# Performance work log

Hardware: AMD Instinct MI355X
Metric: run time of the kernel (lower is better)

## Reference

```python
import jax, jax.numpy as jnp
import numpy as np

B, T, QD, KD, E, H, L = 4, 512, 256, 256, 256, 8, 4
DH = E // H
SHAPES = np.array([[64, 64], [32, 32], [16, 16], [8, 8]], dtype=np.int64)
S = int(np.sum(SHAPES[:, 0] * SHAPES[:, 1]))  # 5440


def setup_inputs() -> dict:
    key = jax.random.key(0)
    ks = jax.random.split(key, 16)
    std = 0.02
    return {
        "q": jax.random.normal(ks[0], (B, T, QD), jnp.float32),
        "k": jax.random.normal(ks[1], (B, S, KD), jnp.float32),
        "v": jax.random.normal(ks[2], (B, S, KD), jnp.float32),
        "Wq": jax.random.normal(ks[3], (E, QD), jnp.float32) * std,
        "bq": jnp.zeros((E,), jnp.float32),
        "Wk": jax.random.normal(ks[4], (E, KD), jnp.float32) * std,
        "bk": jnp.zeros((E,), jnp.float32),
        "Wv": jax.random.normal(ks[5], (E, KD), jnp.float32) * std,
        "bv": jnp.zeros((E,), jnp.float32),
        "Wo": jax.random.normal(ks[6], (QD, E), jnp.float32) * std,
        "bo": jnp.zeros((QD,), jnp.float32),
        "Wl": jax.random.normal(ks[7], (H * L, QD), jnp.float32) * std,
        "bl": jnp.zeros((H * L,), jnp.float32),
        "k_spatial_shapes": SHAPES,  # static int metadata (split sizes)
    }


def _heads(x, b):
    # [b, s, E] -> [b, H, s, DH]
    return x.reshape(b, -1, H, DH).transpose(0, 2, 1, 3)


def reference(q, k, v, Wq, bq, Wk, bk, Wv, bv, Wo, bo, Wl, bl, k_spatial_shapes):
    scale = DH ** -0.5
    bsz = q.shape[0]
    # per-head, per-level gate: [B, H, T, L], softmax over levels
    gates = jax.nn.softmax(
        (q @ Wl.T + bl).reshape(bsz, -1, H, L).transpose(0, 2, 1, 3), axis=-1
    )
    qs = _heads((q @ Wq.T + bq) * scale, bsz)   # [B,H,T,DH]
    ks_ = _heads(k @ Wk.T + bk, bsz)            # [B,H,S,DH]
    vs = _heads(v @ Wv.T + bv, bsz)             # [B,H,S,DH]
    scores = jnp.einsum("bhtd,bhsd->bhts", qs, ks_)  # [B,H,T,S]
    sizes = [int(h_ * w_) for h_, w_ in np.asarray(k_spatial_shapes)]
    offs = np.concatenate([[0], np.cumsum(sizes)])
    # segmented softmax per level, weighted by the learned level gate
    pieces = [
        jax.nn.softmax(scores[..., offs[i]:offs[i + 1]], axis=-1) * gates[..., i:i + 1]
        for i in range(len(sizes))
    ]
    attn = jnp.concatenate(pieces, axis=-1)  # [B,H,T,S]
    out = jnp.einsum("bhts,bhsd->bhtd", attn, vs)
    out = out.transpose(0, 2, 1, 3).reshape(bsz, -1, E)
    out = out @ Wo.T + bo
    return out, attn
```

## Files before the change

kernel.cpp:

```cpp
#include <hip/hip_runtime.h>
#include <hip/hip_bf16.h>

#define Bn 4
#define Hn 8
#define Tn 512
#define Sn 5440
#define DHn 32
#define En 256

typedef short bf16x8 __attribute__((ext_vector_type(8)));
typedef float f32x4 __attribute__((ext_vector_type(4)));

static __device__ __forceinline__ unsigned short f2bf(float f) {
    union { float f; unsigned u; } c; c.f = f;
    unsigned r = c.u + 0x7fffu + ((c.u >> 16) & 1u);
    return (unsigned short)(r >> 16);
}

static __device__ __forceinline__ unsigned int cvtpk(float a, float b) {
    __hip_bfloat162 h = __float22bfloat162_rn(make_float2(a, b));
    unsigned int u; __builtin_memcpy(&u, &h, 4); return u;
}

__global__ __launch_bounds__(256) void gates_kernel(
    const float* __restrict__ q, const float* __restrict__ Wl,
    const float* __restrict__ bl, float* __restrict__ gates)
{
    __shared__ float qr[8][256];
    __shared__ float lgs[8][32];
    int tid = threadIdx.x;
    int bt0 = blockIdx.x * 8;

    {
        const float4* src = (const float4*)(q + (size_t)bt0 * 256);
        float4* dst = (float4*)&qr[0][0];
        dst[tid] = src[tid];
        dst[tid + 256] = src[tid + 256];
    }
    __syncthreads();

    int r = tid >> 5, o = tid & 31;
    float acc = 0.f;
    const float4* w4 = (const float4*)(Wl + (size_t)o * 256);
    const float4* q4 = (const float4*)&qr[r][0];
    #pragma unroll 8
    for (int i = 0; i < 64; i++) {
        float4 w = w4[i]; float4 qq = q4[i];
        acc += qq.x*w.x + qq.y*w.y + qq.z*w.z + qq.w*w.w;
    }
    lgs[r][o] = acc + bl[o];
    __syncthreads();

    if (tid < 64) {
        int rr = tid >> 3, h = tid & 7;
        float x0 = lgs[rr][h*4+0], x1 = lgs[rr][h*4+1], x2 = lgs[rr][h*4+2], x3 = lgs[rr][h*4+3];
        float mx = fmaxf(fmaxf(x0,x1), fmaxf(x2,x3));
        float e0 = __expf(x0-mx), e1 = __expf(x1-mx), e2 = __expf(x2-mx), e3 = __expf(x3-mx);
        float inv = 1.f / (e0+e1+e2+e3);
        int bt = bt0 + rr; int b = bt >> 9, t = bt & 511;
        float* g = gates + (((size_t)b*Hn + h)*Tn + t)*4;
        g[0] = e0*inv; g[1] = e1*inv; g[2] = e2*inv; g[3] = e3*inv;
    }
}

static __device__ __forceinline__ void gemm_core(
    const float* __restrict__ A, const float* __restrict__ W,
    int row0, int col0, int tid, int wr, int wc, int lr, int lg,
    unsigned short (*As)[40], unsigned short (*Ws)[40], f32x4 acc[4][4])
{
    for (int k0 = 0; k0 < 256; k0 += 32) {
        __syncthreads();
        #pragma unroll
        for (int i = 0; i < 4; i++) {
            int f4 = tid + i*256;
            int r = f4 >> 3, kc = (f4 & 7) * 4;
            float4 v = *(const float4*)(A + (size_t)(row0 + r)*256 + k0 + kc);
            uint2 pk; pk.x = cvtpk(v.x, v.y); pk.y = cvtpk(v.z, v.w);
            *(uint2*)&As[r][kc] = pk;
        }
        #pragma unroll
        for (int i = 0; i < 4; i++) {
            int f4 = tid + i*256;
            int r = f4 >> 3, kc = (f4 & 7) * 4;
            float4 v = *(const float4*)(W + (size_t)(col0 + r)*256 + k0 + kc);
            uint2 pk; pk.x = cvtpk(v.x, v.y); pk.y = cvtpk(v.z, v.w);
            *(uint2*)&Ws[r][kc] = pk;
        }
        __syncthreads();

        bf16x8 af[4], wf[4];
        #pragma unroll
        for (int i = 0; i < 4; i++) {
            af[i] = *(const bf16x8*)&As[wr*64 + i*16 + lr][lg*8];
            wf[i] = *(const bf16x8*)&Ws[wc*64 + i*16 + lr][lg*8];
        }
        #pragma unroll
        for (int i = 0; i < 4; i++)
            #pragma unroll
            for (int j = 0; j < 4; j++)
                acc[i][j] = __builtin_amdgcn_mfma_f32_16x16x32_bf16(af[i], wf[j], acc[i][j], 0, 0, 0);
    }
}

__global__ __launch_bounds__(256) void proj_kvq(
    const float* __restrict__ kin, const float* __restrict__ Wk, const float* __restrict__ bk,
    const float* __restrict__ vin, const float* __restrict__ Wv, const float* __restrict__ bv,
    const float* __restrict__ qin, const float* __restrict__ Wq, const float* __restrict__ bq,
    unsigned short* __restrict__ ks_out, unsigned short* __restrict__ vt_out,
    unsigned short* __restrict__ qs_out)
{
    int mode = blockIdx.z;
    if (mode == 2 && blockIdx.x >= 16) return;

    __shared__ unsigned short As[128][40];
    __shared__ unsigned short Ws[128][40];

    const float* A    = (mode == 0) ? kin : (mode == 1) ? vin : qin;
    const float* W    = (mode == 0) ? Wk  : (mode == 1) ? Wv  : Wq;
    const float* bias = (mode == 0) ? bk  : (mode == 1) ? bv  : bq;

    int tid = threadIdx.x;
    int l = tid & 63, wid = tid >> 6;
    int wr = wid >> 1, wc = wid & 1;
    int lr = l & 15, lg = l >> 4;
    int row0 = blockIdx.x * 128, col0 = blockIdx.y * 128;

    f32x4 acc[4][4] = {};
    gemm_core(A, W, row0, col0, tid, wr, wc, lr, lg, As, Ws, acc);

    const float qscale = 0.17677669529663687f * 1.4426950408889634f;

    #pragma unroll
    for (int i = 0; i < 4; i++) {
        int m0 = row0 + wr*64 + i*16 + lg*4;
        #pragma unroll
        for (int j = 0; j < 4; j++) {
            int col = col0 + wc*64 + j*16 + lr;
            float bvv = bias[col];
            if (mode == 0) {
                #pragma unroll
                for (int r = 0; r < 4; r++) {
                    int m = m0 + r;
                    int b = m / Sn, s = m - b*Sn;
                    ks_out[(((size_t)b*Hn + (col >> 5))*Sn + s)*DHn + (col & 31)] = f2bf(acc[i][j][r] + bvv);
                }
            } else if (mode == 1) {
                int b = m0 / Sn, s0 = m0 - b*Sn;
                uint2 pk;
                pk.x = cvtpk(acc[i][j][0] + bvv, acc[i][j][1] + bvv);
                pk.y = cvtpk(acc[i][j][2] + bvv, acc[i][j][3] + bvv);
                *(uint2*)&vt_out[(((size_t)b*Hn + (col >> 5))*DHn + (col & 31))*Sn + s0] = pk;
            } else {
                #pragma unroll
                for (int r = 0; r < 4; r++) {
                    int m = m0 + r;
                    int b = m >> 9, t = m & 511;
                    qs_out[(((size_t)b*Hn + (col >> 5))*Tn + t)*DHn + (col & 31)] = f2bf((acc[i][j][r] + bvv) * qscale);
                }
            }
        }
    }
}

__global__ __launch_bounds__(256) void proj_out(
    const float* __restrict__ A, const float* __restrict__ W,
    const float* __restrict__ bias, float* __restrict__ out)
{
    __shared__ unsigned short As[128][40];
    __shared__ unsigned short Ws[128][40];

    int tid = threadIdx.x;
    int l = tid & 63, wid = tid >> 6;
    int wr = wid >> 1, wc = wid & 1;
    int lr = l & 15, lg = l >> 4;
    int row0 = blockIdx.x * 128, col0 = blockIdx.y * 128;

    f32x4 acc[4][4] = {};
    gemm_core(A, W, row0, col0, tid, wr, wc, lr, lg, As, Ws, acc);

    #pragma unroll
    for (int i = 0; i < 4; i++) {
        int m0 = row0 + wr*64 + i*16 + lg*4;
        #pragma unroll
        for (int j = 0; j < 4; j++) {
            int col = col0 + wc*64 + j*16 + lr;
            float bvv = bias[col];
            #pragma unroll
            for (int r = 0; r < 4; r++)
                __builtin_nontemporal_store(acc[i][j][r] + bvv, &out[(size_t)(m0 + r)*256 + col]);
        }
    }
}

__global__ __launch_bounds__(256, 5) void attn_fused(
    const unsigned short* __restrict__ qs, const unsigned short* __restrict__ ks,
    const unsigned short* __restrict__ vt, const float* __restrict__ gates,
    float* __restrict__ attn_out, float* __restrict__ o_tmp)
{
    __shared__ char plds[4][2048];
    __shared__ char estw[4][4096];
    __shared__ float lsum[4][4][16];
    __shared__ float denom[4][16];

    int n = blockIdx.x;
    int bh = ((n >> 8) << 3) | (n & 7);
    int tt = (n >> 3) & 31;
    int t0 = tt << 4;
    int b = bh >> 3, h = bh & 7;
    int tid = threadIdx.x;
    int l = tid & 63, w = tid >> 6;
    int lr = l & 15, lg = l >> 4;

    bf16x8 aq = *(const bf16x8*)(qs + ((size_t)bh*Tn + t0 + lr)*DHn + lg*8);
    const unsigned short* kb = ks + (size_t)bh * Sn * DHn;
    const unsigned short* vb = vt + (size_t)bh * DHn * Sn;
    const f32x4 fzero = {0.f, 0.f, 0.f, 0.f};

    float lp0 = 0.f, lp1 = 0.f, lp2 = 0.f, lp3 = 0.f;
    for (int c = w; c < 85; c += 4) {
        const unsigned short* kc_ = kb + (size_t)c * 64 * DHn;
        bf16x8 kf0 = *(const bf16x8*)(kc_ + (size_t)(lr     )*DHn + lg*8);
        bf16x8 kf1 = *(const bf16x8*)(kc_ + (size_t)(16 + lr)*DHn + lg*8);
        bf16x8 kf2 = *(const bf16x8*)(kc_ + (size_t)(32 + lr)*DHn + lg*8);
        bf16x8 kf3 = *(const bf16x8*)(kc_ + (size_t)(48 + lr)*DHn + lg*8);
        f32x4 s0 = __builtin_amdgcn_mfma_f32_16x16x32_bf16(kf0, aq, fzero, 0, 0, 0);
        f32x4 s1 = __builtin_amdgcn_mfma_f32_16x16x32_bf16(kf1, aq, fzero, 0, 0, 0);
        f32x4 s2 = __builtin_amdgcn_mfma_f32_16x16x32_bf16(kf2, aq, fzero, 0, 0, 0);
        f32x4 s3 = __builtin_amdgcn_mfma_f32_16x16x32_bf16(kf3, aq, fzero, 0, 0, 0);
        float es = exp2f(s0[0]) + exp2f(s0[1]) + exp2f(s0[2]) + exp2f(s0[3])
                 + exp2f(s1[0]) + exp2f(s1[1]) + exp2f(s1[2]) + exp2f(s1[3])
                 + exp2f(s2[0]) + exp2f(s2[1]) + exp2f(s2[2]) + exp2f(s2[3])
                 + exp2f(s3[0]) + exp2f(s3[1]) + exp2f(s3[2]) + exp2f(s3[3]);
        if      (c < 64) lp0 += es;
        else if (c < 80) lp1 += es;
        else if (c < 84) lp2 += es;
        else             lp3 += es;
    }
    {
        float v;
        v = lp0; v += __shfl_xor(v, 16); v += __shfl_xor(v, 32); lp0 = v;
        v = lp1; v += __shfl_xor(v, 16); v += __shfl_xor(v, 32); lp1 = v;
        v = lp2; v += __shfl_xor(v, 16); v += __shfl_xor(v, 32); lp2 = v;
        v = lp3; v += __shfl_xor(v, 16); v += __shfl_xor(v, 32); lp3 = v;
    }
    if (l < 16) {
        lsum[w][0][lr] = lp0; lsum[w][1][lr] = lp1;
        lsum[w][2][lr] = lp2; lsum[w][3][lr] = lp3;
    }
    __syncthreads();
    if (tid < 64) {
        int seg = tid >> 4, row = tid & 15;
        denom[seg][row] = lsum[0][seg][row] + lsum[1][seg][row] + lsum[2][seg][row] + lsum[3][seg][row];
    }
    __syncthreads();

    float lcf0, lcf1, lcf2, lcf3;
    {
        const float* g = gates + ((size_t)bh*Tn + t0 + lr)*4;
        lcf0 = __log2f(g[0] / denom[0][lr]);
        lcf1 = __log2f(g[1] / denom[1][lr]);
        lcf2 = __log2f(g[2] / denom[2][lr]);
        lcf3 = __log2f(g[3] / denom[3][lr]);
    }

    f32x4 acc0 = fzero, acc1 = fzero;
    char* pbase = plds[w];
    char* ebase = estw[w];
    int swz = (lr & 7) << 4;
    float* abase = attn_out + ((size_t)bh*Tn + t0)*Sn;

    for (int c = w; c < 85; c += 4) {
        float lcf = (c < 64) ? lcf0 : (c < 80) ? lcf1 : (c < 84) ? lcf2 : lcf3;

        const unsigned short* kc_ = kb + (size_t)c * 64 * DHn;
        bf16x8 kf0 = *(const bf16x8*)(kc_ + (size_t)(lr     )*DHn + lg*8);
        bf16x8 kf1 = *(const bf16x8*)(kc_ + (size_t)(16 + lr)*DHn + lg*8);
        bf16x8 kf2 = *(const bf16x8*)(kc_ + (size_t)(32 + lr)*DHn + lg*8);
        bf16x8 kf3 = *(const bf16x8*)(kc_ + (size_t)(48 + lr)*DHn + lg*8);
        bf16x8 vf0 = *(const bf16x8*)(vb + (size_t)(lr     )*Sn + c*64      + lg*8);
        bf16x8 vf1 = *(const bf16x8*)(vb + (size_t)(16 + lr)*Sn + c*64      + lg*8);
        bf16x8 vf2 = *(const bf16x8*)(vb + (size_t)(lr     )*Sn + c*64 + 32 + lg*8);
        bf16x8 vf3 = *(const bf16x8*)(vb + (size_t)(16 + lr)*Sn + c*64 + 32 + lg*8);

        f32x4 s0 = __builtin_amdgcn_mfma_f32_16x16x32_bf16(kf0, aq, fzero, 0, 0, 0);
        f32x4 s1 = __builtin_amdgcn_mfma_f32_16x16x32_bf16(kf1, aq, fzero, 0, 0, 0);
        f32x4 s2 = __builtin_amdgcn_mfma_f32_16x16x32_bf16(kf2, aq, fzero, 0, 0, 0);
        f32x4 s3 = __builtin_amdgcn_mfma_f32_16x16x32_bf16(kf3, aq, fzero, 0, 0, 0);

        {
            f32x4 av;
            av[0] = exp2f(s0[0]+lcf); av[1] = exp2f(s0[1]+lcf); av[2] = exp2f(s0[2]+lcf); av[3] = exp2f(s0[3]+lcf);
            *(f32x4*)(ebase + ((lr*256 +   0 + lg*16) ^ swz)) = av;
            uint2 pk; pk.x = cvtpk(av[0], av[1]); pk.y = cvtpk(av[2], av[3]);
            *(uint2*)(pbase + ((lr*128 +   0 + lg*8) ^ swz)) = pk;
            av[0] = exp2f(s1[0]+lcf); av[1] = exp2f(s1[1]+lcf); av[2] = exp2f(s1[2]+lcf); av[3] = exp2f(s1[3]+lcf);
            *(f32x4*)(ebase + ((lr*256 +  64 + lg*16) ^ swz)) = av;
            pk.x = cvtpk(av[0], av[1]); pk.y = cvtpk(av[2], av[3]);
            *(uint2*)(pbase + ((lr*128 +  32 + lg*8) ^ swz)) = pk;
            av[0] = exp2f(s2[0]+lcf); av[1] = exp2f(s2[1]+lcf); av[2] = exp2f(s2[2]+lcf); av[3] = exp2f(s2[3]+lcf);
            *(f32x4*)(ebase + ((lr*256 + 128 + lg*16) ^ swz)) = av;
            pk.x = cvtpk(av[0], av[1]); pk.y = cvtpk(av[2], av[3]);
            *(uint2*)(pbase + ((lr*128 +  64 + lg*8) ^ swz)) = pk;
            av[0] = exp2f(s3[0]+lcf); av[1] = exp2f(s3[1]+lcf); av[2] = exp2f(s3[2]+lcf); av[3] = exp2f(s3[3]+lcf);
            *(f32x4*)(ebase + ((lr*256 + 192 + lg*16) ^ swz)) = av;
            pk.x = cvtpk(av[0], av[1]); pk.y = cvtpk(av[2], av[3]);
            *(uint2*)(pbase + ((lr*128 +  96 + lg*8) ^ swz)) = pk;
        }

        __builtin_amdgcn_s_setprio(1);
        {
            bf16x8 pa0 = *(const bf16x8*)(pbase + ((lr*128 +      lg*16) ^ swz));
            acc0 = __builtin_amdgcn_mfma_f32_16x16x32_bf16(pa0, vf0, acc0, 0, 0, 0);
            acc1 = __builtin_amdgcn_mfma_f32_16x16x32_bf16(pa0, vf1, acc1, 0, 0, 0);
            bf16x8 pa1 = *(const bf16x8*)(pbase + ((lr*128 + 64 + lg*16) ^ swz));
            acc0 = __builtin_amdgcn_mfma_f32_16x16x32_bf16(pa1, vf2, acc0, 0, 0, 0);
            acc1 = __builtin_amdgcn_mfma_f32_16x16x32_bf16(pa1, vf3, acc1, 0, 0, 0);
        }
        __builtin_amdgcn_s_setprio(0);

        #pragma unroll
        for (int i = 0; i < 4; i++) {
            int row = i*4 + lg;
            f32x4 vv = *(const f32x4*)(ebase + ((row*256 + lr*16) ^ ((row & 7) << 4)));
            __builtin_nontemporal_store(vv, (f32x4*)(abase + (size_t)row*Sn + c*64 + lr*4));
        }
    }

    float* ored = (float*)estw[w];
    #pragma unroll
    for (int r = 0; r < 4; r++) {
        ored[(4*lg + r)*32 + lr]      = acc0[r];
        ored[(4*lg + r)*32 + 16 + lr] = acc1[r];
    }
    __syncthreads();
    #pragma unroll
    for (int i = 0; i < 2; i++) {
        int idx = tid + i*256;
        int row = idx >> 5, d = idx & 31;
        float sum = ((float*)estw[0])[row*32 + d] + ((float*)estw[1])[row*32 + d]
                  + ((float*)estw[2])[row*32 + d] + ((float*)estw[3])[row*32 + d];
        __builtin_nontemporal_store(sum, &o_tmp[((size_t)(b*Tn + t0 + row))*En + h*DHn + d]);
    }
}

extern "C" void kernel_launch(void* const* d_in, const int* in_sizes, int n_in,
                              void* d_out, int out_size, void* d_ws, size_t ws_size,
                              hipStream_t stream)
{
    const float* q  = (const float*)d_in[0];
    const float* k  = (const float*)d_in[1];
    const float* v  = (const float*)d_in[2];
    const float* Wq = (const float*)d_in[3];
    const float* bq = (const float*)d_in[4];
    const float* Wk = (const float*)d_in[5];
    const float* bk = (const float*)d_in[6];
    const float* Wv = (const float*)d_in[7];
    const float* bv = (const float*)d_in[8];
    const float* Wo = (const float*)d_in[9];
    const float* bo = (const float*)d_in[10];
    const float* Wl = (const float*)d_in[11];
    const float* bl = (const float*)d_in[12];

    float* out  = (float*)d_out;
    float* attn = out + (size_t)Bn*Tn*256;

    char* ws = (char*)d_ws;
    unsigned short* qs    = (unsigned short*)ws;
    unsigned short* ksb   = (unsigned short*)(ws + (1u<<20));
    unsigned short* vtb   = (unsigned short*)(ws + (1u<<20) + 11141120u);
    float*          gates = (float*)(ws + (1u<<20) + 2u*11141120u);
    float*          o_tmp = (float*)(ws + (1u<<20) + 2u*11141120u + 262144u);

    gates_kernel<<<Bn*Tn/8, 256, 0, stream>>>(q, Wl, bl, gates);
    proj_kvq<<<dim3((Bn*Sn)/128, 2, 3), 256, 0, stream>>>(
        k, Wk, bk, v, Wv, bv, q, Wq, bq, ksb, vtb, qs);
    attn_fused<<<Bn*Hn*(Tn/16), 256, 0, stream>>>(qs, ksb, vtb, gates, attn, o_tmp);
    proj_out<<<dim3((Bn*Tn)/128, 2), 256, 0, stream>>>(o_tmp, Wo, bo, out);
}
```

Measured before the change: 160.8 us.

## Process two 16-row query tiles per block to reuse K/V loads

Each attention block now handles 32 query rows instead of 16, sharing each loaded K and V fragment across two MFMA query tiles. This halves global K/V fragment traffic and halves the grid size. In exchange it doubles LDS staging and register use, drops the occupancy hint from launch bounds, and leaves fewer blocks to spread across CUs.

```diff
diff --git a/kernel.cpp b/kernel.cpp
--- a/kernel.cpp
+++ b/kernel.cpp
@@ -192,85 +192,110 @@
     }
 }
 
-__global__ __launch_bounds__(256, 5) void attn_fused(
+__global__ __launch_bounds__(256) void attn_fused(
     const unsigned short* __restrict__ qs, const unsigned short* __restrict__ ks,
     const unsigned short* __restrict__ vt, const float* __restrict__ gates,
     float* __restrict__ attn_out, float* __restrict__ o_tmp)
 {
-    __shared__ char plds[4][2048];
-    __shared__ char estw[4][4096];
-    __shared__ float lsum[4][4][16];
-    __shared__ float denom[4][16];
+    __shared__ char plds[4][2][2048];
+    __shared__ char estw[4][2][4096];
+    __shared__ float lsum[4][2][4][16];
+    __shared__ float denom[2][4][16];
 
     int n = blockIdx.x;
-    int bh = ((n >> 8) << 3) | (n & 7);
-    int tt = (n >> 3) & 31;
-    int t0 = tt << 4;
+    int xcd = n & 7, j = n >> 3;
+    int bh = ((j >> 4) << 3) | xcd;
+    int t0 = (j & 15) << 5;
     int b = bh >> 3, h = bh & 7;
     int tid = threadIdx.x;
     int l = tid & 63, w = tid >> 6;
     int lr = l & 15, lg = l >> 4;
 
-    bf16x8 aq = *(const bf16x8*)(qs + ((size_t)bh*Tn + t0 + lr)*DHn + lg*8);
+    bf16x8 aqA = *(const bf16x8*)(qs + ((size_t)bh*Tn + t0 + lr)*DHn + lg*8);
+    bf16x8 aqB = *(const bf16x8*)(qs + ((size_t)bh*Tn + t0 + 16 + lr)*DHn + lg*8);
     const unsigned short* kb = ks + (size_t)bh * Sn * DHn;
     const unsigned short* vb = vt + (size_t)bh * DHn * Sn;
     const f32x4 fzero = {0.f, 0.f, 0.f, 0.f};
 
-    float lp0 = 0.f, lp1 = 0.f, lp2 = 0.f, lp3 = 0.f;
+    float lpA0 = 0.f, lpA1 = 0.f, lpA2 = 0.f, lpA3 = 0.f;
+    float lpB0 = 0.f, lpB1 = 0.f, lpB2 = 0.f, lpB3 = 0.f;
     for (int c = w; c < 85; c += 4) {
         const unsigned short* kc_ = kb + (size_t)c * 64 * DHn;
         bf16x8 kf0 = *(const bf16x8*)(kc_ + (size_t)(lr     )*DHn + lg*8);
         bf16x8 kf1 = *(const bf16x8*)(kc_ + (size_t)(16 + lr)*DHn + lg*8);
         bf16x8 kf2 = *(const bf16x8*)(kc_ + (size_t)(32 + lr)*DHn + lg*8);
         bf16x8 kf3 = *(const bf16x8*)(kc_ + (size_t)(48 + lr)*DHn + lg*8);
-        f32x4 s0 = __builtin_amdgcn_mfma_f32_16x16x32_bf16(kf0, aq, fzero, 0, 0, 0);
-        f32x4 s1 = __builtin_amdgcn_mfma_f32_16x16x32_bf16(kf1, aq, fzero, 0, 0, 0);
-        f32x4 s2 = __builtin_amdgcn_mfma_f32_16x16x32_bf16(kf2, aq, fzero, 0, 0, 0);
-        f32x4 s3 = __builtin_amdgcn_mfma_f32_16x16x32_bf16(kf3, aq, fzero, 0, 0, 0);
-        float es = exp2f(s0[0]) + exp2f(s0[1]) + exp2f(s0[2]) + exp2f(s0[3])
-                 + exp2f(s1[0]) + exp2f(s1[1]) + exp2f(s1[2]) + exp2f(s1[3])
-                 + exp2f(s2[0]) + exp2f(s2[1]) + exp2f(s2[2]) + exp2f(s2[3])
-                 + exp2f(s3[0]) + exp2f(s3[1]) + exp2f(s3[2]) + exp2f(s3[3]);
-        if      (c < 64) lp0 += es;
-        else if (c < 80) lp1 += es;
-        else if (c < 84) lp2 += es;
-        else             lp3 += es;
+        f32x4 sA0 = __builtin_amdgcn_mfma_f32_16x16x32_bf16(kf0, aqA, fzero, 0, 0, 0);
+        f32x4 sA1 = __builtin_amdgcn_mfma_f32_16x16x32_bf16(kf1, aqA, fzero, 0, 0, 0);
+        f32x4 sA2 = __builtin_amdgcn_mfma_f32_16x16x32_bf16(kf2, aqA, fzero, 0, 0, 0);
+        f32x4 sA3 = __builtin_amdgcn_mfma_f32_16x16x32_bf16(kf3, aqA, fzero, 0, 0, 0);
+        f32x4 sB0 = __builtin_amdgcn_mfma_f32_16x16x32_bf16(kf0, aqB, fzero, 0, 0, 0);
+        f32x4 sB1 = __builtin_amdgcn_mfma_f32_16x16x32_bf16(kf1, aqB, fzero, 0, 0, 0);
+        f32x4 sB2 = __builtin_amdgcn_mfma_f32_16x16x32_bf16(kf2, aqB, fzero, 0, 0, 0);
+        f32x4 sB3 = __builtin_amdgcn_mfma_f32_16x16x32_bf16(kf3, aqB, fzero, 0, 0, 0);
+        float esA = exp2f(sA0[0]) + exp2f(sA0[1]) + exp2f(sA0[2]) + exp2f(sA0[3])
+                  + exp2f(sA1[0]) + exp2f(sA1[1]) + exp2f(sA1[2]) + exp2f(sA1[3])
+                  + exp2f(sA2[0]) + exp2f(sA2[1]) + exp2f(sA2[2]) + exp2f(sA2[3])
+                  + exp2f(sA3[0]) + exp2f(sA3[1]) + exp2f(sA3[2]) + exp2f(sA3[3]);
+        float esB = exp2f(sB0[0]) + exp2f(sB0[1]) + exp2f(sB0[2]) + exp2f(sB0[3])
+                  + exp2f(sB1[0]) + exp2f(sB1[1]) + exp2f(sB1[2]) + exp2f(sB1[3])
+                  + exp2f(sB2[0]) + exp2f(sB2[1]) + exp2f(sB2[2]) + exp2f(sB2[3])
+                  + exp2f(sB3[0]) + exp2f(sB3[1]) + exp2f(sB3[2]) + exp2f(sB3[3]);
+        if      (c < 64) { lpA0 += esA; lpB0 += esB; }
+        else if (c < 80) { lpA1 += esA; lpB1 += esB; }
+        else if (c < 84) { lpA2 += esA; lpB2 += esB; }
+        else             { lpA3 += esA; lpB3 += esB; }
     }
     {
         float v;
-        v = lp0; v += __shfl_xor(v, 16); v += __shfl_xor(v, 32); lp0 = v;
-        v = lp1; v += __shfl_xor(v, 16); v += __shfl_xor(v, 32); lp1 = v;
-        v = lp2; v += __shfl_xor(v, 16); v += __shfl_xor(v, 32); lp2 = v;
-        v = lp3; v += __shfl_xor(v, 16); v += __shfl_xor(v, 32); lp3 = v;
+        v = lpA0; v += __shfl_xor(v, 16); v += __shfl_xor(v, 32); lpA0 = v;
+        v = lpA1; v += __shfl_xor(v, 16); v += __shfl_xor(v, 32); lpA1 = v;
+        v = lpA2; v += __shfl_xor(v, 16); v += __shfl_xor(v, 32); lpA2 = v;
+        v = lpA3; v += __shfl_xor(v, 16); v += __shfl_xor(v, 32); lpA3 = v;
+        v = lpB0; v += __shfl_xor(v, 16); v += __shfl_xor(v, 32); lpB0 = v;
+        v = lpB1; v += __shfl_xor(v, 16); v += __shfl_xor(v, 32); lpB1 = v;
+        v = lpB2; v += __shfl_xor(v, 16); v += __shfl_xor(v, 32); lpB2 = v;
+        v = lpB3; v += __shfl_xor(v, 16); v += __shfl_xor(v, 32); lpB3 = v;
     }
     if (l < 16) {
-        lsum[w][0][lr] = lp0; lsum[w][1][lr] = lp1;
-        lsum[w][2][lr] = lp2; lsum[w][3][lr] = lp3;
+        lsum[w][0][0][lr] = lpA0; lsum[w][0][1][lr] = lpA1;
+        lsum[w][0][2][lr] = lpA2; lsum[w][0][3][lr] = lpA3;
+        lsum[w][1][0][lr] = lpB0; lsum[w][1][1][lr] = lpB1;
+        lsum[w][1][2][lr] = lpB2; lsum[w][1][3][lr] = lpB3;
     }
     __syncthreads();
-    if (tid < 64) {
-        int seg = tid >> 4, row = tid & 15;
-        denom[seg][row] = lsum[0][seg][row] + lsum[1][seg][row] + lsum[2][seg][row] + lsum[3][seg][row];
+    if (tid < 128) {
+        int rg = tid >> 6, seg = (tid >> 4) & 3, row = tid & 15;
+        denom[rg][seg][row] = lsum[0][rg][seg][row] + lsum[1][rg][seg][row]
+                            + lsum[2][rg][seg][row] + lsum[3][rg][seg][row];
     }
     __syncthreads();
 
-    float lcf0, lcf1, lcf2, lcf3;
+    float lcfA0, lcfA1, lcfA2, lcfA3, lcfB0, lcfB1, lcfB2, lcfB3;
     {
-        const float* g = gates + ((size_t)bh*Tn + t0 + lr)*4;
-        lcf0 = __log2f(g[0] / denom[0][lr]);
-        lcf1 = __log2f(g[1] / denom[1][lr]);
-        lcf2 = __log2f(g[2] / denom[2][lr]);
-        lcf3 = __log2f(g[3] / denom[3][lr]);
-    }
-
-    f32x4 acc0 = fzero, acc1 = fzero;
-    char* pbase = plds[w];
-    char* ebase = estw[w];
+        const float* gA = gates + ((size_t)bh*Tn + t0 + lr)*4;
+        const float* gB = gates + ((size_t)bh*Tn + t0 + 16 + lr)*4;
+        lcfA0 = __log2f(gA[0] / denom[0][0][lr]);
+        lcfA1 = __log2f(gA[1] / denom[0][1][lr]);
+        lcfA2 = __log2f(gA[2] / denom[0][2][lr]);
+        lcfA3 = __log2f(gA[3] / denom[0][3][lr]);
+        lcfB0 = __log2f(gB[0] / denom[1][0][lr]);
+        lcfB1 = __log2f(gB[1] / denom[1][1][lr]);
+        lcfB2 = __log2f(gB[2] / denom[1][2][lr]);
+        lcfB3 = __log2f(gB[3] / denom[1][3][lr]);
+    }
+
+    f32x4 accA0 = fzero, accA1 = fzero, accB0 = fzero, accB1 = fzero;
+    char* pA = plds[w][0];
+    char* pB = plds[w][1];
+    char* eA = estw[w][0];
+    char* eB = estw[w][1];
     int swz = (lr & 7) << 4;
     float* abase = attn_out + ((size_t)bh*Tn + t0)*Sn;
 
     for (int c = w; c < 85; c += 4) {
-        float lcf = (c < 64) ? lcf0 : (c < 80) ? lcf1 : (c < 84) ? lcf2 : lcf3;
+        float lcfA = (c < 64) ? lcfA0 : (c < 80) ? lcfA1 : (c < 84) ? lcfA2 : lcfA3;
+        float lcfB = (c < 64) ? lcfB0 : (c < 80) ? lcfB1 : (c < 84) ? lcfB2 : lcfB3;
 
         const unsigned short* kc_ = kb + (size_t)c * 64 * DHn;
         bf16x8 kf0 = *(const bf16x8*)(kc_ + (size_t)(lr     )*DHn + lg*8);
@@ -282,59 +307,93 @@
         bf16x8 vf2 = *(const bf16x8*)(vb + (size_t)(lr     )*Sn + c*64 + 32 + lg*8);
         bf16x8 vf3 = *(const bf16x8*)(vb + (size_t)(16 + lr)*Sn + c*64 + 32 + lg*8);
 
-        f32x4 s0 = __builtin_amdgcn_mfma_f32_16x16x32_bf16(kf0, aq, fzero, 0, 0, 0);
-        f32x4 s1 = __builtin_amdgcn_mfma_f32_16x16x32_bf16(kf1, aq, fzero, 0, 0, 0);
-        f32x4 s2 = __builtin_amdgcn_mfma_f32_16x16x32_bf16(kf2, aq, fzero, 0, 0, 0);
-        f32x4 s3 = __builtin_amdgcn_mfma_f32_16x16x32_bf16(kf3, aq, fzero, 0, 0, 0);
+        f32x4 sA0 = __builtin_amdgcn_mfma_f32_16x16x32_bf16(kf0, aqA, fzero, 0, 0, 0);
+        f32x4 sA1 = __builtin_amdgcn_mfma_f32_16x16x32_bf16(kf1, aqA, fzero, 0, 0, 0);
+        f32x4 sA2 = __builtin_amdgcn_mfma_f32_16x16x32_bf16(kf2, aqA, fzero, 0, 0, 0);
+        f32x4 sA3 = __builtin_amdgcn_mfma_f32_16x16x32_bf16(kf3, aqA, fzero, 0, 0, 0);
+        f32x4 sB0 = __builtin_amdgcn_mfma_f32_16x16x32_bf16(kf0, aqB, fzero, 0, 0, 0);
+        f32x4 sB1 = __builtin_amdgcn_mfma_f32_16x16x32_bf16(kf1, aqB, fzero, 0, 0, 0);
+        f32x4 sB2 = __builtin_amdgcn_mfma_f32_16x16x32_bf16(kf2, aqB, fzero, 0, 0, 0);
+        f32x4 sB3 = __builtin_amdgcn_mfma_f32_16x16x32_bf16(kf3, aqB, fzero, 0, 0, 0);
 
         {
             f32x4 av;
-            av[0] = exp2f(s0[0]+lcf); av[1] = exp2f(s0[1]+lcf); av[2] = exp2f(s0[2]+lcf); av[3] = exp2f(s0[3]+lcf);
-            *(f32x4*)(ebase + ((lr*256 +   0 + lg*16) ^ swz)) = av;
+            av[0] = exp2f(sA0[0]+lcfA); av[1] = exp2f(sA0[1]+lcfA); av[2] = exp2f(sA0[2]+lcfA); av[3] = exp2f(sA0[3]+lcfA);
+            *(f32x4*)(eA + ((lr*256 +   0 + lg*16) ^ swz)) = av;
             uint2 pk; pk.x = cvtpk(av[0], av[1]); pk.y = cvtpk(av[2], av[3]);
-            *(uint2*)(pbase + ((lr*128 +   0 + lg*8) ^ swz)) = pk;
-            av[0] = exp2f(s1[0]+lcf); av[1] = exp2f(s1[1]+lcf); av[2] = exp2f(s1[2]+lcf); av[3] = exp2f(s1[3]+lcf);
-            *(f32x4*)(ebase + ((lr*256 +  64 + lg*16) ^ swz)) = av;
-            pk.x = cvtpk(av[0], av[1]); pk.y = cvtpk(av[2], av[3]);
-            *(uint2*)(pbase + ((lr*128 +  32 + lg*8) ^ swz)) = pk;
-            av[0] = exp2f(s2[0]+lcf); av[1] = exp2f(s2[1]+lcf); av[2] = exp2f(s2[2]+lcf); av[3] = exp2f(s2[3]+lcf);
-            *(f32x4*)(ebase + ((lr*256 + 128 + lg*16) ^ swz)) = av;
-            pk.x = cvtpk(av[0], av[1]); pk.y = cvtpk(av[2], av[3]);
-            *(uint2*)(pbase + ((lr*128 +  64 + lg*8) ^ swz)) = pk;
-            av[0] = exp2f(s3[0]+lcf); av[1] = exp2f(s3[1]+lcf); av[2] = exp2f(s3[2]+lcf); av[3] = exp2f(s3[3]+lcf);
-            *(f32x4*)(ebase + ((lr*256 + 192 + lg*16) ^ swz)) = av;
-            pk.x = cvtpk(av[0], av[1]); pk.y = cvtpk(av[2], av[3]);
-            *(uint2*)(pbase + ((lr*128 +  96 + lg*8) ^ swz)) = pk;
+            *(uint2*)(pA + ((lr*128 +   0 + lg*8) ^ swz)) = pk;
+            av[0] = exp2f(sA1[0]+lcfA); av[1] = exp2f(sA1[1]+lcfA); av[2] = exp2f(sA1[2]+lcfA); av[3] = exp2f(sA1[3]+lcfA);
+            *(f32x4*)(eA + ((lr*256 +  64 + lg*16) ^ swz)) = av;
+            pk.x = cvtpk(av[0], av[1]); pk.y = cvtpk(av[2], av[3]);
+            *(uint2*)(pA + ((lr*128 +  32 + lg*8) ^ swz)) = pk;
+            av[0] = exp2f(sA2[0]+lcfA); av[1] = exp2f(sA2[1]+lcfA); av[2] = exp2f(sA2[2]+lcfA); av[3] = exp2f(sA2[3]+lcfA);
+            *(f32x4*)(eA + ((lr*256 + 128 + lg*16) ^ swz)) = av;
+            pk.x = cvtpk(av[0], av[1]); pk.y = cvtpk(av[2], av[3]);
+            *(uint2*)(pA + ((lr*128 +  64 + lg*8) ^ swz)) = pk;
+            av[0] = exp2f(sA3[0]+lcfA); av[1] = exp2f(sA3[1]+lcfA); av[2] = exp2f(sA3[2]+lcfA); av[3] = exp2f(sA3[3]+lcfA);
+            *(f32x4*)(eA + ((lr*256 + 192 + lg*16) ^ swz)) = av;
+            pk.x = cvtpk(av[0], av[1]); pk.y = cvtpk(av[2], av[3]);
+            *(uint2*)(pA + ((lr*128 +  96 + lg*8) ^ swz)) = pk;
+        }
+        {
+            f32x4 av;
+            av[0] = exp2f(sB0[0]+lcfB); av[1] = exp2f(sB0[1]+lcfB); av[2] = exp2f(sB0[2]+lcfB); av[3] = exp2f(sB0[3]+lcfB);
+            *(f32x4*)(eB + ((lr*256 +   0 + lg*16) ^ swz)) = av;
+            uint2 pk; pk.x = cvtpk(av[0], av[1]); pk.y = cvtpk(av[2], av[3]);
+            *(uint2*)(pB + ((lr*128 +   0 + lg*8) ^ swz)) = pk;
+            av[0] = exp2f(sB1[0]+lcfB); av[1] = exp2f(sB1[1]+lcfB); av[2] = exp2f(sB1[2]+lcfB); av[3] = exp2f(sB1[3]+lcfB);
+            *(f32x4*)(eB + ((lr*256 +  64 + lg*16) ^ swz)) = av;
+            pk.x = cvtpk(av[0], av[1]); pk.y = cvtpk(av[2], av[3]);
+            *(uint2*)(pB + ((lr*128 +  32 + lg*8) ^ swz)) = pk;
+            av[0] = exp2f(sB2[0]+lcfB); av[1] = exp2f(sB2[1]+lcfB); av[2] = exp2f(sB2[2]+lcfB); av[3] = exp2f(sB2[3]+lcfB);
+            *(f32x4*)(eB + ((lr*256 + 128 + lg*16) ^ swz)) = av;
+            pk.x = cvtpk(av[0], av[1]); pk.y = cvtpk(av[2], av[3]);
+            *(uint2*)(pB + ((lr*128 +  64 + lg*8) ^ swz)) = pk;
+            av[0] = exp2f(sB3[0]+lcfB); av[1] = exp2f(sB3[1]+lcfB); av[2] = exp2f(sB3[2]+lcfB); av[3] = exp2f(sB3[3]+lcfB);
+            *(f32x4*)(eB + ((lr*256 + 192 + lg*16) ^ swz)) = av;
+            pk.x = cvtpk(av[0], av[1]); pk.y = cvtpk(av[2], av[3]);
+            *(uint2*)(pB + ((lr*128 +  96 + lg*8) ^ swz)) = pk;
         }
 
         __builtin_amdgcn_s_setprio(1);
         {
-            bf16x8 pa0 = *(const bf16x8*)(pbase + ((lr*128 +      lg*16) ^ swz));
-            acc0 = __builtin_amdgcn_mfma_f32_16x16x32_bf16(pa0, vf0, acc0, 0, 0, 0);
-            acc1 = __builtin_amdgcn_mfma_f32_16x16x32_bf16(pa0, vf1, acc1, 0, 0, 0);
-            bf16x8 pa1 = *(const bf16x8*)(pbase + ((lr*128 + 64 + lg*16) ^ swz));
-            acc0 = __builtin_amdgcn_mfma_f32_16x16x32_bf16(pa1, vf2, acc0, 0, 0, 0);
-            acc1 = __builtin_amdgcn_mfma_f32_16x16x32_bf16(pa1, vf3, acc1, 0, 0, 0);
+            bf16x8 paA0 = *(const bf16x8*)(pA + ((lr*128 +      lg*16) ^ swz));
+            accA0 = __builtin_amdgcn_mfma_f32_16x16x32_bf16(paA0, vf0, accA0, 0, 0, 0);
+            accA1 = __builtin_amdgcn_mfma_f32_16x16x32_bf16(paA0, vf1, accA1, 0, 0, 0);
+            bf16x8 paA1 = *(const bf16x8*)(pA + ((lr*128 + 64 + lg*16) ^ swz));
+            accA0 = __builtin_amdgcn_mfma_f32_16x16x32_bf16(paA1, vf2, accA0, 0, 0, 0);
+            accA1 = __builtin_amdgcn_mfma_f32_16x16x32_bf16(paA1, vf3, accA1, 0, 0, 0);
+            bf16x8 paB0 = *(const bf16x8*)(pB + ((lr*128 +      lg*16) ^ swz));
+            accB0 = __builtin_amdgcn_mfma_f32_16x16x32_bf16(paB0, vf0, accB0, 0, 0, 0);
+            accB1 = __builtin_amdgcn_mfma_f32_16x16x32_bf16(paB0, vf1, accB1, 0, 0, 0);
+            bf16x8 paB1 = *(const bf16x8*)(pB + ((lr*128 + 64 + lg*16) ^ swz));
+            accB0 = __builtin_amdgcn_mfma_f32_16x16x32_bf16(paB1, vf2, accB0, 0, 0, 0);
+            accB1 = __builtin_amdgcn_mfma_f32_16x16x32_bf16(paB1, vf3, accB1, 0, 0, 0);
         }
         __builtin_amdgcn_s_setprio(0);
 
         #pragma unroll
         for (int i = 0; i < 4; i++) {
             int row = i*4 + lg;
-            f32x4 vv = *(const f32x4*)(ebase + ((row*256 + lr*16) ^ ((row & 7) << 4)));
-            __builtin_nontemporal_store(vv, (f32x4*)(abase + (size_t)row*Sn + c*64 + lr*4));
+            f32x4 vvA = *(const f32x4*)(eA + ((row*256 + lr*16) ^ ((row & 7) << 4)));
+            __builtin_nontemporal_store(vvA, (f32x4*)(abase + (size_t)row*Sn + c*64 + lr*4));
+            f32x4 vvB = *(const f32x4*)(eB + ((row*256 + lr*16) ^ ((row & 7) << 4)));
+            __builtin_nontemporal_store(vvB, (f32x4*)(abase + (size_t)(16 + row)*Sn + c*64 + lr*4));
         }
     }
 
     float* ored = (float*)estw[w];
     #pragma unroll
     for (int r = 0; r < 4; r++) {
-        ored[(4*lg + r)*32 + lr]      = acc0[r];
-        ored[(4*lg + r)*32 + 16 + lr] = acc1[r];
+        int row = 4*lg + r;
+        ored[row*32 + lr]             = accA0[r];
+        ored[row*32 + 16 + lr]        = accA1[r];
+        ored[(16 + row)*32 + lr]      = accB0[r];
+        ored[(16 + row)*32 + 16 + lr] = accB1[r];
     }
     __syncthreads();
     #pragma unroll
-    for (int i = 0; i < 2; i++) {
+    for (int i = 0; i < 4; i++) {
         int idx = tid + i*256;
         int row = idx >> 5, d = idx & 31;
         float sum = ((float*)estw[0])[row*32 + d] + ((float*)estw[1])[row*32 + d]
@@ -374,6 +433,6 @@
     gates_kernel<<<Bn*Tn/8, 256, 0, stream>>>(q, Wl, bl, gates);
     proj_kvq<<<dim3((Bn*Sn)/128, 2, 3), 256, 0, stream>>>(
         k, Wk, bk, v, Wv, bv, q, Wq, bq, ksb, vtb, qs);
-    attn_fused<<<Bn*Hn*(Tn/16), 256, 0, stream>>>(qs, ksb, vtb, gates, attn, o_tmp);
+    attn_fused<<<512, 256, 0, stream>>>(qs, ksb, vtb, gates, attn, o_tmp);
     proj_out<<<dim3((Bn*Tn)/128, 2), 256, 0, stream>>>(o_tmp, Wo, bo, out);
 }
```

Result: no change. 158.8 us (-1.3%).
